# Performance work log

Measured on AMD Instinct MI355X. Metric: run time of the kernel, lower is better.

## Reference

```python
import jax, jax.numpy as jnp
import numpy as np

NUM_GROUPS = 4
NUM_HEADS = 4
EPS = 1e-6

def group_norm(x, scale, bias):
    # x: [B, C, L]
    b, c, l = x.shape
    g = NUM_GROUPS
    xg = x.reshape(b, g, (c // g) * l)
    mean = xg.mean(axis=-1, keepdims=True)
    var = xg.var(axis=-1, keepdims=True)
    xg = (xg - mean) * jax.lax.rsqrt(var + EPS)
    xn = xg.reshape(b, c, l)
    return xn * scale[None, :, None] + bias[None, :, None]

def conv1x1(x, w, b):
    # x: [B, C_in, L], w: [C_out, C_in], b: [C_out]
    return jnp.einsum('oc,bcl->bol', w, x) + b[None, :, None]

def setup_inputs() -> dict:
    key = jax.random.key(0)
    ks = jax.random.split(key, 11)
    B, C, L = 8, 512, 2048
    x = jax.random.normal(ks[0], (B, C, L), dtype=jnp.float32)
    s = 1.0 / np.sqrt(C)
    return {
        'x': x,
        'gn_scale': jnp.ones((C,), jnp.float32),
        'gn_bias': jnp.zeros((C,), jnp.float32),
        'wq': jax.random.normal(ks[1], (C, C), jnp.float32) * s,
        'bq': jnp.zeros((C,), jnp.float32),
        'wk': jax.random.normal(ks[2], (C, C), jnp.float32) * s,
        'bk': jnp.zeros((C,), jnp.float32),
        'wv': jax.random.normal(ks[3], (C, C), jnp.float32) * s,
        'bv': jnp.zeros((C,), jnp.float32),
        'wo': jax.random.normal(ks[4], (C, C), jnp.float32) * s,
        'bo': jnp.zeros((C,), jnp.float32),
    }

def reference(x, gn_scale, gn_bias, wq, bq, wk, bk, wv, bv, wo, bo):
    b, c, l = x.shape
    nh = NUM_HEADS
    hd = c // nh
    h_ = group_norm(x, gn_scale, gn_bias)
    q = conv1x1(h_, wq, bq).reshape(b, nh, hd, l)
    k = conv1x1(h_, wk, bk).reshape(b, nh, hd, l)
    v = conv1x1(h_, wv, bv).reshape(b, nh, hd, l)
    # scores: [b, nh, l(query), l(key)]
    w_ = jnp.einsum('bhdq,bhdk->bhqk', q, k) * (hd ** -0.5)
    w_ = jax.nn.softmax(w_, axis=-1)
    # attn: [b, nh, l(query), hd]
    attn = jnp.einsum('bhqk,bhdk->bhqd', w_, v)
    attn = attn.transpose(0, 1, 3, 2).reshape(b, c, l)
    out = conv1x1(attn, wo, bo)
    return x + out
```

## Files before the change

kernel.cpp:

```cpp
#include <hip/hip_runtime.h>


typedef unsigned short u16;
typedef unsigned int   u32;
typedef unsigned long long u64;
typedef __attribute__((ext_vector_type(8)))  short          bf16x8;
typedef __attribute__((ext_vector_type(4)))  float          f32x4;
typedef __attribute__((ext_vector_type(4)))  unsigned int   u32x4;
typedef __attribute__((ext_vector_type(8)))  unsigned short u16x8;

#define MFMA16(a, b, c) __builtin_amdgcn_mfma_f32_16x16x32_bf16((a), (b), (c), 0, 0, 0)

#define WAIT_VM6         3958
#define WAIT_VM4_LGKM0    116
#define BARRIER() __builtin_amdgcn_s_barrier()

__device__ __forceinline__ u16 f2bf(float f) {
    union { float f; unsigned int i; } cv;
    cv.f = f;
    unsigned int u = cv.i;
    u += 0x7fffu + ((u >> 16) & 1);
    return (u16)(u >> 16);
}
__device__ __forceinline__ u32 fbits(float f) {
    union { float f; unsigned int i; } cv; cv.f = f; return cv.i;
}

__device__ __forceinline__ void async16(const u16* g, u16* l) {
    __builtin_amdgcn_global_load_lds(
        (const __attribute__((address_space(1))) unsigned int*)g,
        (__attribute__((address_space(3))) unsigned int*)l, 16, 0, 0);
}

#define BATCH 8
#define CCH   512
#define LEN   2048
#define NGRP  4
#define NHEAD 4
#define HD    128
#define GSIZE (128 * 2048)

__global__ __launch_bounds__(256) void prep_k(const float* __restrict__ x,
                                              float* __restrict__ stats,
                                              const float* __restrict__ w0,
                                              const float* __restrict__ w1,
                                              const float* __restrict__ w2,
                                              const float* __restrict__ w3,
                                              u16* __restrict__ dst) {
    const int bid = blockIdx.x;
    if (bid < 256) {
        const int grp   = bid >> 3;
        const int chunk = bid & 7;
        const int b = grp >> 2, g = grp & 3;
        const float* base = x + ((size_t)(b * CCH + g * 128 + chunk * 16)) * LEN;

        float s = 0.f, ss = 0.f;
        for (int i = 0; i < 32; ++i) {
            int cid = threadIdx.x + i * 256;
            f32x4 dv = *(const f32x4*)(base + (size_t)cid * 4);
            for (int u = 0; u < 4; ++u) { s += dv[u]; ss += dv[u] * dv[u]; }
        }
        for (int m = 1; m < 64; m <<= 1) {
            s  += __shfl_xor(s,  m, 64);
            ss += __shfl_xor(ss, m, 64);
        }
        __shared__ float red[8];
        int wid = threadIdx.x >> 6, lane = threadIdx.x & 63;
        if (lane == 0) { red[wid * 2] = s; red[wid * 2 + 1] = ss; }
        __syncthreads();
        if (threadIdx.x == 0) {
            float ts  = red[0] + red[2] + red[4] + red[6];
            float tss = red[1] + red[3] + red[5] + red[7];
            atomicAdd(&stats[grp * 2],     ts);
            atomicAdd(&stats[grp * 2 + 1], tss);
        }
    } else {
        const int wb = bid - 256;
        const int mat = wb >> 7, chunk = wb & 127;
        const float* src = (mat == 0) ? w0 : (mat == 1) ? w1 : (mat == 2) ? w2 : w3;
        const size_t base = (size_t)chunk * 2048 + (size_t)threadIdx.x * 8;
        f32x4 a = *(const f32x4*)(src + base);
        f32x4 b2 = *(const f32x4*)(src + base + 4);
        u16x8 o;
        for (int u = 0; u < 4; ++u) { o[u] = f2bf(a[u]); o[u + 4] = f2bf(b2[u]); }
        *(u16x8*)(dst + (size_t)mat * 262144 + base) = o;
    }
}

__global__ __launch_bounds__(256) void gn_apply_k(const float* __restrict__ x,
                                                  const float* __restrict__ gns,
                                                  const float* __restrict__ gnb,
                                                  const float* __restrict__ stats,
                                                  u16* __restrict__ hT) {
    __shared__ u16 Ts[64 * 72];
    const int b = blockIdx.z, c0 = blockIdx.y * 64, l0 = blockIdx.x * 64;
    const int g = c0 >> 7;
    const int tid = threadIdx.x;

    float sum   = stats[(b * NGRP + g) * 2];
    float sumsq = stats[(b * NGRP + g) * 2 + 1];
    const float invN = 1.f / (float)GSIZE;
    float mean = sum * invN;
    float var  = sumsq * invN - mean * mean;
    float rstd = rsqrtf(var + 1e-6f);

    for (int i = 0; i < 4; ++i) {
        int cid = tid + i * 256;
        int row = cid >> 4, c4 = cid & 15;
        int c = c0 + row;
        float sc = gns[c] * rstd;
        float bi = gnb[c] - mean * sc;
        f32x4 dv = *(const f32x4*)(x + ((size_t)(b * CCH + c)) * LEN + l0 + c4 * 4);
        for (int u = 0; u < 4; ++u)
            Ts[row * 72 + c4 * 4 + u] = f2bf(dv[u] * sc + bi);
    }
    __syncthreads();
    for (int i = 0; i < 2; ++i) {
        int cid = tid + i * 256;
        int lrow = cid >> 3, c8 = cid & 7;
        u16x8 ov;
        for (int u = 0; u < 8; ++u) ov[u] = Ts[(c8 * 8 + u) * 72 + lrow];
        *(u16x8*)(hT + ((size_t)b * LEN + l0 + lrow) * CCH + c0 + c8 * 8) = ov;
    }
}

__global__ __launch_bounds__(256, 2) void gemm01_k(const u16* __restrict__ hT,
                                                   const u16* __restrict__ wq_bf,
                                                   const u16* __restrict__ wk_bf,
                                                   const u16* __restrict__ wv_bf,
                                                   const float* __restrict__ bq,
                                                   const float* __restrict__ bk,
                                                   const float* __restrict__ bv,
                                                   u16* __restrict__ qT,
                                                   u16* __restrict__ kT,
                                                   u16* __restrict__ vbuf) {
    __shared__ u16 As[2][128 * 64];
    __shared__ u16 Bs[2][128 * 64];
    const int bid = blockIdx.x;
    const bool mode0 = (bid < 1024);
    int b, m0, n0;
    const u16 *Arow, *Brow;
    if (mode0) {
        b = bid >> 7; m0 = ((bid >> 3) & 15) * 128; n0 = (bid & 7) * 128;
        Arow = hT + ((size_t)b * LEN + m0) * 512;
        Brow = (n0 < 512) ? (wq_bf + (size_t)n0 * 512)
                          : (wk_bf + (size_t)(n0 - 512) * 512);
    } else {
        int bid2 = bid - 1024;
        b = bid2 >> 6; m0 = ((bid2 >> 4) & 3) * 128; n0 = (bid2 & 15) * 128;
        Arow = wv_bf + (size_t)m0 * 512;
        Brow = hT + ((size_t)b * LEN + n0) * 512;
    }

    const int tid = threadIdx.x;
    const int lane = tid & 63, wid = tid >> 6;
    const int quad = lane >> 4, l15 = lane & 15;
    const int wm = (wid & 1) * 64, wn = (wid >> 1) * 64;

    f32x4 acc[4][4] = {};
    const int srl = lane >> 3, scl = lane & 7;

#pragma unroll
    for (int i = 0; i < 4; ++i) {
        int rloc = wid * 32 + i * 8 + srl;
        int lc = scl ^ (rloc & 7);
        async16(Arow + (size_t)rloc * 512 + lc * 8, &As[0][(wid * 32 + i * 8) * 64]);
        async16(Brow + (size_t)rloc * 512 + lc * 8, &Bs[0][(wid * 32 + i * 8) * 64]);
    }
    __syncthreads();

    for (int kk = 0; kk < 8; ++kk) {
        const int p = kk & 1;
        if (kk < 7) {
            const int k0n = (kk + 1) * 64;
#pragma unroll
            for (int i = 0; i < 4; ++i) {
                int rloc = wid * 32 + i * 8 + srl;
                int lc = scl ^ (rloc & 7);
                async16(Arow + (size_t)rloc * 512 + k0n + lc * 8,
                        &As[1 - p][(wid * 32 + i * 8) * 64]);
                async16(Brow + (size_t)rloc * 512 + k0n + lc * 8,
                        &Bs[1 - p][(wid * 32 + i * 8) * 64]);
            }
        }
#pragma unroll
        for (int ks = 0; ks < 2; ++ks) {
            bf16x8 af[4], bfr[4];
            for (int t = 0; t < 4; ++t) {
                int ra = wm + t * 16 + l15, rb = wn + t * 16 + l15;
                af[t]  = *(const bf16x8*)(&As[p][ra * 64 + (((ks * 4 + quad) ^ (ra & 7))) * 8]);
                bfr[t] = *(const bf16x8*)(&Bs[p][rb * 64 + (((ks * 4 + quad) ^ (rb & 7))) * 8]);
            }
            for (int mt = 0; mt < 4; ++mt)
                for (int nt = 0; nt < 4; ++nt)
                    acc[mt][nt] = MFMA16(af[mt], bfr[nt], acc[mt][nt]);
        }
        __syncthreads();
    }

    if (mode0) {
        const int col0 = (n0 < 512) ? n0 : n0 - 512;
        const float* biasp = ((n0 < 512) ? bq : bk) + col0;
        u16* outp = (n0 < 512) ? qT : kT;
        for (int nt = 0; nt < 4; ++nt) {
            int nl = wn + nt * 16 + l15;
            float bv_ = biasp[nl];
            for (int mt = 0; mt < 4; ++mt)
                for (int r = 0; r < 4; ++r) {
                    int ml = wm + mt * 16 + quad * 4 + r;
                    size_t idx = ((size_t)b * LEN + m0 + ml) * 512 + col0 + nl;
                    outp[idx] = f2bf(acc[mt][nt][r] + bv_);
                }
        }
    } else {
        for (int mt = 0; mt < 4; ++mt)
            for (int r = 0; r < 4; ++r) {
                int ml = wm + mt * 16 + quad * 4 + r;
                float bv_ = bv[m0 + ml];
                for (int nt = 0; nt < 4; ++nt) {
                    int nl = wn + nt * 16 + l15;
                    size_t idx = ((size_t)(b * 512 + m0 + ml)) * LEN + n0 + nl;
                    vbuf[idx] = f2bf(acc[mt][nt][r] + bv_);
                }
            }
    }
}

__global__ __launch_bounds__(256, 2) void gemm2_k(const u16* __restrict__ A0,
                                                  const u16* __restrict__ B0,
                                                  const float* __restrict__ bias0,
                                                  const float* __restrict__ resid,
                                                  float* __restrict__ out0) {
    __shared__ u16 As[2][128 * 64];
    __shared__ u16 Bs[2][128 * 64];
    const int b  = blockIdx.z;
    const int n0 = blockIdx.x * 128;
    const int m0 = blockIdx.y * 128;
    const int tid = threadIdx.x;
    const int lane = tid & 63, wid = tid >> 6;
    const int quad = lane >> 4, l15 = lane & 15;
    const int wm = (wid & 1) * 64, wn = (wid >> 1) * 64;

    const u16* Arow = A0 + (size_t)m0 * 512;
    const u16* Brow = B0 + ((size_t)b * LEN + n0) * 512;

    f32x4 acc[4][4] = {};
    const int srl = lane >> 3, scl = lane & 7;

#pragma unroll
    for (int i = 0; i < 4; ++i) {
        int rloc = wid * 32 + i * 8 + srl;
        int lc = scl ^ (rloc & 7);
        async16(Arow + (size_t)rloc * 512 + lc * 8, &As[0][(wid * 32 + i * 8) * 64]);
        async16(Brow + (size_t)rloc * 512 + lc * 8, &Bs[0][(wid * 32 + i * 8) * 64]);
    }
    __syncthreads();

    for (int kk = 0; kk < 8; ++kk) {
        const int p = kk & 1;
        if (kk < 7) {
            const int k0n = (kk + 1) * 64;
#pragma unroll
            for (int i = 0; i < 4; ++i) {
                int rloc = wid * 32 + i * 8 + srl;
                int lc = scl ^ (rloc & 7);
                async16(Arow + (size_t)rloc * 512 + k0n + lc * 8,
                        &As[1 - p][(wid * 32 + i * 8) * 64]);
                async16(Brow + (size_t)rloc * 512 + k0n + lc * 8,
                        &Bs[1 - p][(wid * 32 + i * 8) * 64]);
            }
        }
#pragma unroll
        for (int ks = 0; ks < 2; ++ks) {
            bf16x8 af[4], bfr[4];
            for (int t = 0; t < 4; ++t) {
                int ra = wm + t * 16 + l15, rb = wn + t * 16 + l15;
                af[t]  = *(const bf16x8*)(&As[p][ra * 64 + (((ks * 4 + quad) ^ (ra & 7))) * 8]);
                bfr[t] = *(const bf16x8*)(&Bs[p][rb * 64 + (((ks * 4 + quad) ^ (rb & 7))) * 8]);
            }
            for (int mt = 0; mt < 4; ++mt)
                for (int nt = 0; nt < 4; ++nt)
                    acc[mt][nt] = MFMA16(af[mt], bfr[nt], acc[mt][nt]);
        }
        __syncthreads();
    }

    for (int mt = 0; mt < 4; ++mt)
        for (int r = 0; r < 4; ++r) {
            int ml = wm + mt * 16 + quad * 4 + r;
            float bv_ = bias0[m0 + ml];
            for (int nt = 0; nt < 4; ++nt) {
                int nl = wn + nt * 16 + l15;
                size_t idx = ((size_t)(b * 512 + m0 + ml)) * LEN + n0 + nl;
                out0[idx] = acc[mt][nt][r] + bv_ + resid[idx];
            }
        }
}

__global__ __launch_bounds__(512, 4) void attn_k(const u16* __restrict__ qT,
                                                 const u16* __restrict__ kT,
                                                 const u16* __restrict__ v,
                                                 u16* __restrict__ attnT) {
    __shared__ u16 Ks[2][64 * 128];
    __shared__ u16 Vs[2][128 * 64];
    const int bid = blockIdx.x;
    const int xcd = bid & 7, slot = bid >> 3;
    const int bh  = xcd * 4 + (slot >> 4);
    const int qt  = slot & 15;
    const int b = bh >> 2, h = bh & 3;
    const int i0 = qt * 128;

    const int tid = threadIdx.x, lane = tid & 63, wid = tid >> 6;
    const int quad = lane >> 4, l15 = lane & 15;
    const int mrow = wid * 16 + l15;

    bf16x8 qa[4];
    for (int ks = 0; ks < 4; ++ks)
        qa[ks] = *(const bf16x8*)(qT + ((size_t)b * LEN + i0 + mrow) * 512 + h * HD +
                                  ks * 32 + quad * 8);

    float mst = -3.0e38f, lst = 0.f;
    f32x4 oacc[8] = {};

    const float SL2E = 0.08838834764831845f * 1.4426950408889634f;

    const u16* kbase = kT + ((size_t)b * LEN) * 512 + h * HD;
    const u16* vbase = v + ((size_t)(b * CCH + h * HD)) * LEN;

    const u16* kgp[2];
    const u16* vgp[2];
    int krow[2], vrow[2];
#pragma unroll
    for (int i = 0; i < 2; ++i) {
        int rk = wid * 8 + i * 4 + (lane >> 4);
        krow[i] = wid * 8 + i * 4;
        kgp[i] = kbase + (size_t)rk * 512 + ((lane & 15) ^ (rk & 7)) * 8;
        int rv = wid * 16 + i * 8 + (lane >> 3);
        vrow[i] = wid * 16 + i * 8;
        vgp[i] = vbase + (size_t)rv * LEN + ((lane & 7) ^ (rv & 7)) * 8;
    }

#pragma unroll
    for (int i = 0; i < 2; ++i) {
        async16(kgp[i], &Ks[0][krow[i] * 128]);
        async16(vgp[i], &Vs[0][vrow[i] * 64]);
        kgp[i] += 64 * 512;
        vgp[i] += 64;
    }

    for (int jt = 0; jt < 32; ++jt) {
        const int p = jt & 1;

#pragma unroll
        for (int i = 0; i < 2; ++i) {
            async16(kgp[i], &Ks[1 - p][krow[i] * 128]);
            async16(vgp[i], &Vs[1 - p][vrow[i] * 64]);
        }
        if (jt < 30) {
#pragma unroll
            for (int i = 0; i < 2; ++i) { kgp[i] += 64 * 512; vgp[i] += 64; }
        }

        __builtin_amdgcn_s_waitcnt(WAIT_VM6);
        BARRIER();

        f32x4 st[4] = {};
#pragma unroll
        for (int jtn = 0; jtn < 4; ++jtn) {
            int r = jtn * 16 + l15;
            for (int ks = 0; ks < 4; ++ks) {
                bf16x8 kf = *(const bf16x8*)(&Ks[p][r * 128 + ((ks * 4 + quad) ^ (r & 7)) * 8]);
                st[jtn] = MFMA16(kf, qa[ks], st[jtn]);
            }
        }

        float rm = -3.0e38f;
        for (int jtn = 0; jtn < 4; ++jtn)
            for (int r = 0; r < 4; ++r) rm = fmaxf(rm, st[jtn][r]);
        rm *= SL2E;
        rm = fmaxf(rm, __shfl_xor(rm, 16, 64));
        rm = fmaxf(rm, __shfl_xor(rm, 32, 64));
        float mnew  = fmaxf(mst, rm);
        float alpha = __builtin_amdgcn_exp2f(mst - mnew);
        mst = mnew;
        float rs = 0.f;
        for (int jtn = 0; jtn < 4; ++jtn)
            for (int r = 0; r < 4; ++r) {
                float pv_ = __builtin_amdgcn_exp2f(st[jtn][r] * SL2E - mnew);
                st[jtn][r] = pv_;
                rs += pv_;
            }
        rs += __shfl_xor(rs, 16, 64);
        rs += __shfl_xor(rs, 32, 64);
        lst = lst * alpha + rs;

        if (__ballot(alpha != 1.0f) != 0ull) {
            float av[4];
            for (int r = 0; r < 4; ++r) av[r] = __shfl(alpha, quad * 4 + r, 16);
            for (int dt = 0; dt < 8; ++dt)
                for (int r = 0; r < 4; ++r) oacc[dt][r] *= av[r];
        }

        __builtin_amdgcn_s_waitcnt(WAIT_VM4_LGKM0);
        BARRIER();

        {
            int m = mrow;
#pragma unroll
            for (int jtn = 0; jtn < 4; ++jtn) {
                u64 packed =  (u64)((fbits(st[jtn][0]) + 0x8000u) >> 16)
                           | ((u64)((fbits(st[jtn][1]) + 0x8000u) >> 16) << 16)
                           | ((u64)((fbits(st[jtn][2]) + 0x8000u) >> 16) << 32)
                           | ((u64)((fbits(st[jtn][3]) + 0x8000u) >> 16) << 48);
                int pc = (jtn * 2 + (quad >> 1)) ^ (m & 7);
                *(u64*)(&Ks[p][m * 64 + pc * 8 + (quad & 1) * 4]) = packed;
            }
        }

#pragma unroll
        for (int ks = 0; ks < 2; ++ks) {
            bf16x8 pf = *(const bf16x8*)(&Ks[p][mrow * 64 + ((ks * 4 + quad) ^ (mrow & 7)) * 8]);
            for (int dt = 0; dt < 8; ++dt) {
                int d = dt * 16 + l15;
                bf16x8 vf = *(const bf16x8*)(&Vs[p][d * 64 + ((ks * 4 + quad) ^ (d & 7)) * 8]);
                oacc[dt] = MFMA16(pf, vf, oacc[dt]);
            }
        }

        __builtin_amdgcn_s_waitcnt(WAIT_VM4_LGKM0);
        BARRIER();
    }

    float inv = 1.f / lst;
    float iv[4];
    for (int r = 0; r < 4; ++r) iv[r] = __shfl(inv, quad * 4 + r, 16);
    for (int r = 0; r < 4; ++r) {
        int m = i0 + wid * 16 + quad * 4 + r;
        for (int dt = 0; dt < 8; ++dt) {
            int d = dt * 16 + l15;
            attnT[((size_t)b * LEN + m) * 512 + h * HD + d] = f2bf(oacc[dt][r] * iv[r]);
        }
    }
}

extern "C" void kernel_launch(void* const* d_in, const int* in_sizes, int n_in,
                              void* d_out, int out_size, void* d_ws, size_t ws_size,
                              hipStream_t stream) {
    const float* x   = (const float*)d_in[0];
    const float* gns = (const float*)d_in[1];
    const float* gnb = (const float*)d_in[2];
    const float* wq  = (const float*)d_in[3];
    const float* bq  = (const float*)d_in[4];
    const float* wk  = (const float*)d_in[5];
    const float* bk  = (const float*)d_in[6];
    const float* wv  = (const float*)d_in[7];
    const float* bv  = (const float*)d_in[8];
    const float* wo  = (const float*)d_in[9];
    const float* bo  = (const float*)d_in[10];
    float* out = (float*)d_out;

    const size_t NEL = (size_t)BATCH * CCH * LEN;
    float* stats = (float*)d_ws;
    u16* wcat  = (u16*)((char*)d_ws + 256);
    u16* hT    = wcat + 4 * 262144;
    u16* qT    = hT + NEL;
    u16* kT    = qT + NEL;
    u16* vbuf  = kT + NEL;
    u16* attnT = hT;

    const u16* wq_bf = wcat;
    const u16* wk_bf = wcat + 262144;
    const u16* wv_bf = wcat + 2 * 262144;
    const u16* wo_bf = wcat + 3 * 262144;

    hipMemsetAsync(d_ws, 0, 256, stream);
    prep_k<<<768, 256, 0, stream>>>(x, stats, wq, wk, wv, wo, wcat);
    gn_apply_k<<<dim3(32, 8, 8), 256, 0, stream>>>(x, gns, gnb, stats, hT);
    gemm01_k<<<1536, 256, 0, stream>>>(hT, wq_bf, wk_bf, wv_bf, bq, bk, bv, qT, kT, vbuf);
    attn_k<<<512, 512, 0, stream>>>(qT, kT, vbuf, attnT);
    gemm2_k<<<dim3(16, 4, 8), 256, 0, stream>>>(wo_bf, attnT, bo, x, out);
}
```

Before: 268.8 us.

## Switch attention kernel to 32x32x16 MFMA with 4 waves of 32 query rows

Rewrites the flash-attention kernel to use 32x32x16 bf16 MFMA instead of 16x16x32, with 256-thread blocks where each wave owns 32 query rows instead of 16. This cuts one cross-lane shuffle step in the softmax reductions, removes the alpha broadcast shuffles since each lane holds a full row, and lets the output be stored as packed 64-bit writes. Each thread now issues twice as many async K/V loads, and the wait counts are adjusted to match. The trade-off is higher register pressure and fewer waves per block to hide latency.

```diff
diff --git a/kernel.cpp b/kernel.cpp
--- a/kernel.cpp
+++ b/kernel.cpp
@@ -6,13 +6,18 @@
 typedef unsigned long long u64;
 typedef __attribute__((ext_vector_type(8)))  short          bf16x8;
 typedef __attribute__((ext_vector_type(4)))  float          f32x4;
+typedef __attribute__((ext_vector_type(16))) float          f32x16;
 typedef __attribute__((ext_vector_type(4)))  unsigned int   u32x4;
 typedef __attribute__((ext_vector_type(8)))  unsigned short u16x8;
 
 #define MFMA16(a, b, c) __builtin_amdgcn_mfma_f32_16x16x32_bf16((a), (b), (c), 0, 0, 0)
-
+#define MFMA32(a, b, c) __builtin_amdgcn_mfma_f32_32x32x16_bf16((a), (b), (c), 0, 0, 0)
+
+#define WAIT_VM12        3964
+#define WAIT_VM8_LGKM0    120
 #define WAIT_VM6         3958
 #define WAIT_VM4_LGKM0    116
+#define WAIT_LGKM0      49279
 #define BARRIER() __builtin_amdgcn_s_barrier()
 
 __device__ __forceinline__ u16 f2bf(float f) {
@@ -297,7 +302,7 @@
         }
 }
 
-__global__ __launch_bounds__(512, 4) void attn_k(const u16* __restrict__ qT,
+__global__ __launch_bounds__(256, 2) void attn_k(const u16* __restrict__ qT,
                                                  const u16* __restrict__ kT,
                                                  const u16* __restrict__ v,
                                                  u16* __restrict__ attnT) {
@@ -310,38 +315,38 @@
     const int b = bh >> 2, h = bh & 3;
     const int i0 = qt * 128;
 
-    const int tid = threadIdx.x, lane = tid & 63, wid = tid >> 6;
-    const int quad = lane >> 4, l15 = lane & 15;
-    const int mrow = wid * 16 + l15;
-
-    bf16x8 qa[4];
-    for (int ks = 0; ks < 4; ++ks)
+    const int tid = threadIdx.x, lane = tid & 63, wg = tid >> 6;
+    const int l31 = lane & 31, half = lane >> 5;
+    const int mrow = wg * 32 + l31;
+
+    bf16x8 qa[8];
+#pragma unroll
+    for (int ks = 0; ks < 8; ++ks)
         qa[ks] = *(const bf16x8*)(qT + ((size_t)b * LEN + i0 + mrow) * 512 + h * HD +
-                                  ks * 32 + quad * 8);
+                                  ks * 16 + half * 8);
 
     float mst = -3.0e38f, lst = 0.f;
-    f32x4 oacc[8] = {};
+    f32x16 oacc[4] = {};
 
     const float SL2E = 0.08838834764831845f * 1.4426950408889634f;
 
     const u16* kbase = kT + ((size_t)b * LEN) * 512 + h * HD;
     const u16* vbase = v + ((size_t)(b * CCH + h * HD)) * LEN;
-
-    const u16* kgp[2];
-    const u16* vgp[2];
-    int krow[2], vrow[2];
-#pragma unroll
-    for (int i = 0; i < 2; ++i) {
-        int rk = wid * 8 + i * 4 + (lane >> 4);
-        krow[i] = wid * 8 + i * 4;
+    const u16* kgp[4];
+    const u16* vgp[4];
+    int krow[4], vrow[4];
+#pragma unroll
+    for (int i = 0; i < 4; ++i) {
+        int rk = wg * 16 + i * 4 + (lane >> 4);
+        krow[i] = wg * 16 + i * 4;
         kgp[i] = kbase + (size_t)rk * 512 + ((lane & 15) ^ (rk & 7)) * 8;
-        int rv = wid * 16 + i * 8 + (lane >> 3);
-        vrow[i] = wid * 16 + i * 8;
+        int rv = wg * 32 + i * 8 + (lane >> 3);
+        vrow[i] = wg * 32 + i * 8;
         vgp[i] = vbase + (size_t)rv * LEN + ((lane & 7) ^ (rv & 7)) * 8;
     }
 
 #pragma unroll
-    for (int i = 0; i < 2; ++i) {
+    for (int i = 0; i < 4; ++i) {
         async16(kgp[i], &Ks[0][krow[i] * 128]);
         async16(vgp[i], &Vs[0][vrow[i] * 64]);
         kgp[i] += 64 * 512;
@@ -352,95 +357,93 @@
         const int p = jt & 1;
 
 #pragma unroll
-        for (int i = 0; i < 2; ++i) {
-            async16(kgp[i], &Ks[1 - p][krow[i] * 128]);
-            async16(vgp[i], &Vs[1 - p][vrow[i] * 64]);
-        }
+        for (int i = 0; i < 4; ++i) async16(kgp[i], &Ks[1 - p][krow[i] * 128]);
+#pragma unroll
+        for (int i = 0; i < 4; ++i) async16(vgp[i], &Vs[1 - p][vrow[i] * 64]);
         if (jt < 30) {
 #pragma unroll
-            for (int i = 0; i < 2; ++i) { kgp[i] += 64 * 512; vgp[i] += 64; }
-        }
-
-        __builtin_amdgcn_s_waitcnt(WAIT_VM6);
+            for (int i = 0; i < 4; ++i) { kgp[i] += 64 * 512; vgp[i] += 64; }
+        }
+
+        __builtin_amdgcn_s_waitcnt(WAIT_VM12);
         BARRIER();
 
-        f32x4 st[4] = {};
-#pragma unroll
-        for (int jtn = 0; jtn < 4; ++jtn) {
-            int r = jtn * 16 + l15;
-            for (int ks = 0; ks < 4; ++ks) {
-                bf16x8 kf = *(const bf16x8*)(&Ks[p][r * 128 + ((ks * 4 + quad) ^ (r & 7)) * 8]);
-                st[jtn] = MFMA16(kf, qa[ks], st[jtn]);
+        f32x16 st[2] = {};
+#pragma unroll
+        for (int t = 0; t < 2; ++t) {
+            int r = t * 32 + l31;
+            for (int ks = 0; ks < 8; ++ks) {
+                bf16x8 kf = *(const bf16x8*)(&Ks[p][r * 128 + ((ks * 2 + half) ^ (r & 7)) * 8]);
+                st[t] = MFMA32(kf, qa[ks], st[t]);
             }
         }
 
         float rm = -3.0e38f;
-        for (int jtn = 0; jtn < 4; ++jtn)
-            for (int r = 0; r < 4; ++r) rm = fmaxf(rm, st[jtn][r]);
+        for (int t = 0; t < 2; ++t)
+            for (int r = 0; r < 16; ++r) rm = fmaxf(rm, st[t][r]);
         rm *= SL2E;
-        rm = fmaxf(rm, __shfl_xor(rm, 16, 64));
         rm = fmaxf(rm, __shfl_xor(rm, 32, 64));
         float mnew  = fmaxf(mst, rm);
         float alpha = __builtin_amdgcn_exp2f(mst - mnew);
         mst = mnew;
         float rs = 0.f;
-        for (int jtn = 0; jtn < 4; ++jtn)
-            for (int r = 0; r < 4; ++r) {
-                float pv_ = __builtin_amdgcn_exp2f(st[jtn][r] * SL2E - mnew);
-                st[jtn][r] = pv_;
+        for (int t = 0; t < 2; ++t)
+            for (int r = 0; r < 16; ++r) {
+                float pv_ = __builtin_amdgcn_exp2f(st[t][r] * SL2E - mnew);
+                st[t][r] = pv_;
                 rs += pv_;
             }
-        rs += __shfl_xor(rs, 16, 64);
         rs += __shfl_xor(rs, 32, 64);
         lst = lst * alpha + rs;
-
         if (__ballot(alpha != 1.0f) != 0ull) {
-            float av[4];
-            for (int r = 0; r < 4; ++r) av[r] = __shfl(alpha, quad * 4 + r, 16);
-            for (int dt = 0; dt < 8; ++dt)
-                for (int r = 0; r < 4; ++r) oacc[dt][r] *= av[r];
-        }
-
-        __builtin_amdgcn_s_waitcnt(WAIT_VM4_LGKM0);
+            for (int dt = 0; dt < 4; ++dt)
+                for (int r = 0; r < 16; ++r) oacc[dt][r] *= alpha;
+        }
+
+        __builtin_amdgcn_s_waitcnt(WAIT_VM8_LGKM0);
         BARRIER();
 
         {
-            int m = mrow;
-#pragma unroll
-            for (int jtn = 0; jtn < 4; ++jtn) {
-                u64 packed =  (u64)((fbits(st[jtn][0]) + 0x8000u) >> 16)
-                           | ((u64)((fbits(st[jtn][1]) + 0x8000u) >> 16) << 16)
-                           | ((u64)((fbits(st[jtn][2]) + 0x8000u) >> 16) << 32)
-                           | ((u64)((fbits(st[jtn][3]) + 0x8000u) >> 16) << 48);
-                int pc = (jtn * 2 + (quad >> 1)) ^ (m & 7);
-                *(u64*)(&Ks[p][m * 64 + pc * 8 + (quad & 1) * 4]) = packed;
-            }
-        }
-
-#pragma unroll
-        for (int ks = 0; ks < 2; ++ks) {
-            bf16x8 pf = *(const bf16x8*)(&Ks[p][mrow * 64 + ((ks * 4 + quad) ^ (mrow & 7)) * 8]);
-            for (int dt = 0; dt < 8; ++dt) {
-                int d = dt * 16 + l15;
-                bf16x8 vf = *(const bf16x8*)(&Vs[p][d * 64 + ((ks * 4 + quad) ^ (d & 7)) * 8]);
-                oacc[dt] = MFMA16(pf, vf, oacc[dt]);
-            }
-        }
-
-        __builtin_amdgcn_s_waitcnt(WAIT_VM4_LGKM0);
+            u16* Pb = &Ks[p][0];
+#pragma unroll
+            for (int t = 0; t < 2; ++t)
+                for (int g = 0; g < 4; ++g) {
+                    u64 packed =  (u64)((fbits(st[t][g * 4 + 0]) + 0x8000u) >> 16)
+                               | ((u64)((fbits(st[t][g * 4 + 1]) + 0x8000u) >> 16) << 16)
+                               | ((u64)((fbits(st[t][g * 4 + 2]) + 0x8000u) >> 16) << 32)
+                               | ((u64)((fbits(st[t][g * 4 + 3]) + 0x8000u) >> 16) << 48);
+                    int pu = (t * 4 + g) ^ (mrow & 7);
+                    *(u64*)(&Pb[mrow * 64 + pu * 8 + half * 4]) = packed;
+                }
+        }
+
+        {
+            const u16* Pb = &Ks[p][0];
+#pragma unroll
+            for (int jb = 0; jb < 4; ++jb) {
+                bf16x8 pf = *(const bf16x8*)(&Pb[mrow * 64 + ((jb * 2 + half) ^ (mrow & 7)) * 8]);
+                for (int dt = 0; dt < 4; ++dt) {
+                    int d = dt * 32 + l31;
+                    bf16x8 vf = *(const bf16x8*)(&Vs[p][d * 64 + ((jb * 2 + half) ^ (d & 7)) * 8]);
+                    oacc[dt] = MFMA32(vf, pf, oacc[dt]);
+                }
+            }
+        }
+
+        __builtin_amdgcn_s_waitcnt(WAIT_LGKM0);
         BARRIER();
     }
 
     float inv = 1.f / lst;
-    float iv[4];
-    for (int r = 0; r < 4; ++r) iv[r] = __shfl(inv, quad * 4 + r, 16);
-    for (int r = 0; r < 4; ++r) {
-        int m = i0 + wid * 16 + quad * 4 + r;
-        for (int dt = 0; dt < 8; ++dt) {
-            int d = dt * 16 + l15;
-            attnT[((size_t)b * LEN + m) * 512 + h * HD + d] = f2bf(oacc[dt][r] * iv[r]);
-        }
-    }
+    for (int dt = 0; dt < 4; ++dt)
+        for (int g = 0; g < 4; ++g) {
+            u64 w =  (u64)f2bf(oacc[dt][g * 4 + 0] * inv)
+                  | ((u64)f2bf(oacc[dt][g * 4 + 1] * inv) << 16)
+                  | ((u64)f2bf(oacc[dt][g * 4 + 2] * inv) << 32)
+                  | ((u64)f2bf(oacc[dt][g * 4 + 3] * inv) << 48);
+            int c = h * HD + dt * 32 + g * 8 + half * 4;
+            *(u64*)(attnT + ((size_t)b * LEN + i0 + mrow) * 512 + c) = w;
+        }
 }
 
 extern "C" void kernel_launch(void* const* d_in, const int* in_sizes, int n_in,
@@ -477,6 +480,6 @@
     prep_k<<<768, 256, 0, stream>>>(x, stats, wq, wk, wv, wo, wcat);
     gn_apply_k<<<dim3(32, 8, 8), 256, 0, stream>>>(x, gns, gnb, stats, hT);
     gemm01_k<<<1536, 256, 0, stream>>>(hT, wq_bf, wk_bf, wv_bf, bq, bk, bv, qT, kT, vbuf);
-    attn_k<<<512, 512, 0, stream>>>(qT, kT, vbuf, attnT);
+    attn_k<<<512, 256, 0, stream>>>(qT, kT, vbuf, attnT);
     gemm2_k<<<dim3(16, 4, 8), 256, 0, stream>>>(wo_bf, attnT, bo, x, out);
 }
```

Result: faster. 262.3 us (-2.4%).
